# Optimization experiments

Measured on AMD Instinct MI355X. Metric: run time of the kernel, lower is better.

## Reference

```python
import jax, jax.numpy as jnp
import numpy as np

SCOPE = 27
IN_CHANNELS = 512
RICKER_WIDTH = 4.0
DAMP = 0.12
N, H, W = 16, 56, 56


def mexican_hat(scope, width, damping, self_connect=False):
    # Ricker (mexican hat) wavelet sampled at integer offsets around the center.
    t = jnp.arange(scope, dtype=jnp.float32) - (scope - 1) / 2.0
    norm = 2.0 / (np.sqrt(3.0 * width) * np.pi ** 0.25)
    w = damping * norm * (1.0 - (t / width) ** 2) * jnp.exp(-(t ** 2) / (2.0 * width ** 2))
    if not self_connect:
        w = w.at[scope // 2].set(0.0)  # zero self-connection at the center tap
    return w


def setup_inputs() -> dict:
    key = jax.random.key(0)
    activations = jax.random.normal(key, (N, IN_CHANNELS, H, W), dtype=jnp.float32)
    inhibition_filter = mexican_hat(SCOPE, RICKER_WIDTH, DAMP, self_connect=False)
    return {"activations": activations, "inhibition_filter": inhibition_filter}


def reference(activations, inhibition_filter):
    # Converged inhibition: solve y = x + k (circ-conv over channels) y, i.e.
    # y = F^-1( F(x) / F(delta - k_padded) ), FFT taken along the channel axis.
    C = activations.shape[1]
    scope = inhibition_filter.shape[0]
    # pad_roll: zero-pad the scope-length kernel to C taps, then roll so the
    # kernel center sits at circular position 0.
    k = jnp.pad(inhibition_filter, (0, C - scope))
    k = jnp.roll(k, -(scope // 2))
    delta = jnp.zeros((C,), dtype=activations.dtype).at[0].set(1.0)
    fk = jnp.fft.fft(delta - k)                      # complex [C]
    fx = jnp.fft.fft(activations, axis=1)            # complex [N,C,H,W]
    y = jnp.fft.ifft(fx / fk[None, :, None, None], axis=1).real
    return y.astype(activations.dtype)
```

## Files before the change

kernel.cpp:

```cpp
#include <hip/hip_runtime.h>
#include <cstdint>
#include <cstddef>

#define CCH   512
#define FSCOPE 27
#define HWSP  3136
#define NBATCH 16
#define NCOL  (NBATCH*HWSP)

#define BM 128
#define BN 128
#define BK 64
#define NKT (CCH/BK)

#define PI_F 3.14159265358979323846f

typedef __bf16 bf16x8 __attribute__((ext_vector_type(8)));
typedef float  f32x4  __attribute__((ext_vector_type(4)));

static __device__ __forceinline__ unsigned short f2bf(float f) {
  unsigned u = __builtin_bit_cast(unsigned, f);
  unsigned r = 0x7FFFu + ((u >> 16) & 1u);
  return (unsigned short)((u + r) >> 16);
}

__global__ __launch_bounds__(512)
void k_h2(const float* __restrict__ w, float* __restrict__ h) {
  __shared__ float red[8];
  const int d = blockIdx.x;
  const int m = threadIdx.x;

  float re = 1.0f, im = 0.0f;
  #pragma unroll
  for (int j = 0; j < FSCOPE; ++j) {
    int t = (m * (j - FSCOPE/2)) % CCH;
    if (t < 0) t += CCH;
    float ang = (2.0f * PI_F / CCH) * (float)t;
    float s, c;
    sincosf(ang, &s, &c);
    float wj = w[j];
    re -= wj * c;
    im += wj * s;
  }

  int t = (m * d) & (CCH - 1);
  float ang = (2.0f * PI_F / CCH) * (float)t;
  float s, c;
  sincosf(ang, &s, &c);
  float inv = 1.0f / (re * re + im * im);
  float term = (c * re + s * im) * inv;

  #pragma unroll
  for (int off = 32; off > 0; off >>= 1)
    term += __shfl_down(term, off, 64);

  const int lane = m & 63, wv = m >> 6;
  if (lane == 0) red[wv] = term;
  __syncthreads();
  if (m == 0) {
    float tot = 0.f;
    #pragma unroll
    for (int i = 0; i < 8; ++i) tot += red[i];
    h[d] = tot / (float)CCH;
  }
}

__global__ void k_buildH(const float* __restrict__ h, unsigned short* __restrict__ Hm) {
  int m = blockIdx.x;
  for (int k = threadIdx.x; k < CCH; k += blockDim.x) {
    Hm[m*CCH + k] = f2bf(h[(m - k) & (CCH - 1)]);
  }
}

__global__ __launch_bounds__(256, 4)
void k_gemm(const float* __restrict__ X, const unsigned short* __restrict__ Hm,
            float* __restrict__ Y) {
  __shared__ __align__(16) unsigned char lds[BM*BK*2 + BN*BK*2];

  const int tid  = threadIdx.x;
  const int lane = tid & 63;
  const int w    = tid >> 6;

  int bid = blockIdx.x;
  int cpx = gridDim.x >> 3;
  int swz = (bid & 7) * cpx + (bid >> 3);
  const int tm = swz & 3;
  const int tc = swz >> 2;

  const int m0 = tm * BM;
  const int j0 = tc * BN;

  unsigned char* Al = lds;
  unsigned char* Bl = lds + BM*BK*2;

  const int fg = tid & 31;
  const int kg = tid >> 5;
  const int jb = j0 + fg*4;
  const int nb = jb / HWSP;
  const int sb = jb - nb * HWSP;
  const float* Xb = X + (size_t)nb * (CCH*(size_t)HWSP) + sb;

  int wrOff[4];
  #pragma unroll
  for (int c = 0; c < 4; ++c) {
    int col = fg*4 + c;
    int g = (col & 7) ^ ((col >> 3) & 7);
    wrOff[c] = col*128 + (((kg ^ g) & 7) << 4);
  }

  const int wr = w >> 1, wc = w & 1;
  int aBase[4], aSw[4], bBase[4], bSw[4];
  #pragma unroll
  for (int fm = 0; fm < 4; ++fm) {
    int m = wr*64 + fm*16 + (lane & 15);
    aBase[fm] = m*128;
    aSw[fm]   = (m & 7) << 4;
  }
  #pragma unroll
  for (int fn = 0; fn < 4; ++fn) {
    int col = wc*64 + fn*16 + (lane & 15);
    bBase[fn] = col*128;
    bSw[fn]   = ((col & 7) ^ ((col >> 3) & 7)) << 4;
  }

  f32x4 acc[4][4];
  #pragma unroll
  for (int i = 0; i < 4; ++i)
    #pragma unroll
    for (int j = 0; j < 4; ++j)
      acc[i][j] = (f32x4){0.f, 0.f, 0.f, 0.f};

  for (int kt = 0; kt < NKT; ++kt) {
    float4 bv[8];
    const float* Xk = Xb + (size_t)(kt*BK + kg*8) * HWSP;
    #pragma unroll
    for (int kk = 0; kk < 8; ++kk)
      bv[kk] = *reinterpret_cast<const float4*>(Xk + (size_t)kk * HWSP);

    if (kt > 0) __syncthreads();

    #pragma unroll
    for (int i = 0; i < 4; ++i) {
      int m0w = w*32 + i*8;
      int m   = m0w + (lane >> 3);
      int c   = lane & 7;
      const unsigned short* src =
          Hm + (size_t)(m0 + m) * CCH + kt*BK + 8*(c ^ (m & 7));
      unsigned char* dst = Al + m0w * 128;
      __builtin_amdgcn_global_load_lds(
          (const __attribute__((address_space(1))) void*)src,
          (__attribute__((address_space(3))) void*)dst, 16, 0, 0);
    }

    #pragma unroll
    for (int c = 0; c < 4; ++c) {
      union { __bf16 h[8]; int4 v; } u;
      #pragma unroll
      for (int kk = 0; kk < 8; ++kk) {
        float f = (c==0) ? bv[kk].x : (c==1) ? bv[kk].y : (c==2) ? bv[kk].z : bv[kk].w;
        u.h[kk] = (__bf16)f;
      }
      *reinterpret_cast<int4*>(Bl + wrOff[c]) = u.v;
    }

    __syncthreads();

    #pragma unroll
    for (int ks = 0; ks < 2; ++ks) {
      const int kbyte = ks*64 + ((lane >> 4) << 4);
      bf16x8 af[4], bfr[4];
      #pragma unroll
      for (int fm = 0; fm < 4; ++fm)
        af[fm] = *reinterpret_cast<const bf16x8*>(Al + aBase[fm] + (kbyte ^ aSw[fm]));
      #pragma unroll
      for (int fn = 0; fn < 4; ++fn)
        bfr[fn] = *reinterpret_cast<const bf16x8*>(Bl + bBase[fn] + (kbyte ^ bSw[fn]));
      #pragma unroll
      for (int fm = 0; fm < 4; ++fm)
        #pragma unroll
        for (int fn = 0; fn < 4; ++fn)
          acc[fm][fn] = __builtin_amdgcn_mfma_f32_16x16x32_bf16(
              af[fm], bfr[fn], acc[fm][fn], 0, 0, 0);
    }
  }

  #pragma unroll
  for (int fn = 0; fn < 4; ++fn) {
    int colg = j0 + wc*64 + fn*16 + (lane & 15);
    int n = colg / HWSP;
    int s = colg - n * HWSP;
    float* Yb = Y + (size_t)n * (CCH*(size_t)HWSP) + s;
    #pragma unroll
    for (int fm = 0; fm < 4; ++fm) {
      int mrow = m0 + wr*64 + fm*16 + ((lane >> 4) << 2);
      #pragma unroll
      for (int r = 0; r < 4; ++r)
        Yb[(size_t)(mrow + r) * HWSP] = acc[fm][fn][r];
    }
  }
}

extern "C" void kernel_launch(void* const* d_in, const int* in_sizes, int n_in,
                              void* d_out, int out_size, void* d_ws, size_t ws_size,
                              hipStream_t stream) {
  const float* X = (const float*)d_in[0];
  const float* w = (const float*)d_in[1];
  float* Y = (float*)d_out;

  float* h           = (float*)d_ws;
  unsigned short* Hm = (unsigned short*)((char*)d_ws + 4096);

  k_h2    <<<CCH, 512, 0, stream>>>(w, h);
  k_buildH<<<CCH, 256, 0, stream>>>(h, Hm);

  const int nblk = (CCH/BM) * (NCOL/BN);
  k_gemm  <<<nblk, 256, 0, stream>>>(X, Hm, Y);
}
```

Measured before the change: 65.31 us.

## Double-buffer GEMM LDS tiles with register prefetch of next K-tile

Converts the GEMM main loop to a double-buffered LDS scheme. The next K-tile of both the circulant matrix and the activations is loaded into registers before the current tile's MFMAs run, then stored into the alternate buffer, so there is one barrier per iteration instead of two. The A-tile load changes from global_load_lds direct-to-LDS to register loads followed by swizzled LDS stores. LDS grows to 64KB and the occupancy hint drops from 4 to 2 blocks per CU, trading occupancy-based latency hiding for explicit overlap and adding register pressure.

New measurement: 80.94 us. +23.9%, slower.

```diff
diff --git a/kernel.cpp b/kernel.cpp
--- a/kernel.cpp
+++ b/kernel.cpp
@@ -72,10 +72,10 @@
   }
 }
 
-__global__ __launch_bounds__(256, 4)
+__global__ __launch_bounds__(256, 2)
 void k_gemm(const float* __restrict__ X, const unsigned short* __restrict__ Hm,
             float* __restrict__ Y) {
-  __shared__ __align__(16) unsigned char lds[BM*BK*2 + BN*BK*2];
+  __shared__ __align__(16) unsigned char lds[65536];
 
   const int tid  = threadIdx.x;
   const int lane = tid & 63;
@@ -90,8 +90,10 @@
   const int m0 = tm * BM;
   const int j0 = tc * BN;
 
-  unsigned char* Al = lds;
-  unsigned char* Bl = lds + BM*BK*2;
+  const int ar = tid >> 3;
+  const int ac = tid & 7;
+  const unsigned short* aSrcBase = Hm + (size_t)(m0 + ar) * CCH + ac * 8;
+  const int aWr0 = ar * 128 + ((ac ^ (ar & 7)) << 4);
 
   const int fg = tid & 31;
   const int kg = tid >> 5;
@@ -130,28 +132,20 @@
     for (int j = 0; j < 4; ++j)
       acc[i][j] = (f32x4){0.f, 0.f, 0.f, 0.f};
 
-  for (int kt = 0; kt < NKT; ++kt) {
+  {
+    int4 av[4];
     float4 bv[8];
-    const float* Xk = Xb + (size_t)(kt*BK + kg*8) * HWSP;
+    #pragma unroll
+    for (int i = 0; i < 4; ++i)
+      av[i] = *reinterpret_cast<const int4*>(aSrcBase + (size_t)i * 32 * CCH);
+    const float* Xk = Xb + (size_t)(kg * 8) * HWSP;
     #pragma unroll
     for (int kk = 0; kk < 8; ++kk)
       bv[kk] = *reinterpret_cast<const float4*>(Xk + (size_t)kk * HWSP);
 
-    if (kt > 0) __syncthreads();
-
-    #pragma unroll
-    for (int i = 0; i < 4; ++i) {
-      int m0w = w*32 + i*8;
-      int m   = m0w + (lane >> 3);
-      int c   = lane & 7;
-      const unsigned short* src =
-          Hm + (size_t)(m0 + m) * CCH + kt*BK + 8*(c ^ (m & 7));
-      unsigned char* dst = Al + m0w * 128;
-      __builtin_amdgcn_global_load_lds(
-          (const __attribute__((address_space(1))) void*)src,
-          (__attribute__((address_space(3))) void*)dst, 16, 0, 0);
-    }
-
+    #pragma unroll
+    for (int i = 0; i < 4; ++i)
+      *reinterpret_cast<int4*>(lds + aWr0 + i * 4096) = av[i];
     #pragma unroll
     for (int c = 0; c < 4; ++c) {
       union { __bf16 h[8]; int4 v; } u;
@@ -160,10 +154,32 @@
         float f = (c==0) ? bv[kk].x : (c==1) ? bv[kk].y : (c==2) ? bv[kk].z : bv[kk].w;
         u.h[kk] = (__bf16)f;
       }
-      *reinterpret_cast<int4*>(Bl + wrOff[c]) = u.v;
-    }
-
-    __syncthreads();
+      *reinterpret_cast<int4*>(lds + 32768 + wrOff[c]) = u.v;
+    }
+  }
+  __syncthreads();
+
+  #pragma unroll 2
+  for (int kt = 0; kt < NKT; ++kt) {
+    const int cur   = kt & 1;
+    const int aoffC = cur * 16384;
+    const int boffC = 32768 + cur * 16384;
+    const int aoffN = 16384 - aoffC;
+    const int boffN = 32768 + (16384 - aoffC);
+
+    int4 av[4];
+    float4 bv[8];
+    const bool pf = (kt + 1 < NKT);
+    if (pf) {
+      const unsigned short* as = aSrcBase + (kt + 1) * BK;
+      #pragma unroll
+      for (int i = 0; i < 4; ++i)
+        av[i] = *reinterpret_cast<const int4*>(as + (size_t)i * 32 * CCH);
+      const float* Xk = Xb + (size_t)((kt + 1) * BK + kg * 8) * HWSP;
+      #pragma unroll
+      for (int kk = 0; kk < 8; ++kk)
+        bv[kk] = *reinterpret_cast<const float4*>(Xk + (size_t)kk * HWSP);
+    }
 
     #pragma unroll
     for (int ks = 0; ks < 2; ++ks) {
@@ -171,10 +187,10 @@
       bf16x8 af[4], bfr[4];
       #pragma unroll
       for (int fm = 0; fm < 4; ++fm)
-        af[fm] = *reinterpret_cast<const bf16x8*>(Al + aBase[fm] + (kbyte ^ aSw[fm]));
+        af[fm] = *reinterpret_cast<const bf16x8*>(lds + aoffC + aBase[fm] + (kbyte ^ aSw[fm]));
       #pragma unroll
       for (int fn = 0; fn < 4; ++fn)
-        bfr[fn] = *reinterpret_cast<const bf16x8*>(Bl + bBase[fn] + (kbyte ^ bSw[fn]));
+        bfr[fn] = *reinterpret_cast<const bf16x8*>(lds + boffC + bBase[fn] + (kbyte ^ bSw[fn]));
       #pragma unroll
       for (int fm = 0; fm < 4; ++fm)
         #pragma unroll
@@ -182,6 +198,24 @@
           acc[fm][fn] = __builtin_amdgcn_mfma_f32_16x16x32_bf16(
               af[fm], bfr[fn], acc[fm][fn], 0, 0, 0);
     }
+
+    if (pf) {
+      #pragma unroll
+      for (int i = 0; i < 4; ++i)
+        *reinterpret_cast<int4*>(lds + aoffN + aWr0 + i * 4096) = av[i];
+      #pragma unroll
+      for (int c = 0; c < 4; ++c) {
+        union { __bf16 h[8]; int4 v; } u;
+        #pragma unroll
+        for (int kk = 0; kk < 8; ++kk) {
+          float f = (c==0) ? bv[kk].x : (c==1) ? bv[kk].y : (c==2) ? bv[kk].z : bv[kk].w;
+          u.h[kk] = (__bf16)f;
+        }
+        *reinterpret_cast<int4*>(lds + boffN + wrOff[c]) = u.v;
+      }
+    }
+
+    __syncthreads();
   }
 
   #pragma unroll
```

## Software-pipeline GEMM mainloop with double-buffered A tile and register-prefetched B

Applied to the files above, without the earlier changes.

The GEMM mainloop now prefetches the next K-tile while computing the current one. The Hm (A) tile is loaded directly into a second LDS buffer, and the X (B) values are loaded into registers, then converted to bf16 and written to LDS after the MFMAs. The aim is to hide global-load latency behind compute. In exchange, LDS grows to 48KB and the occupancy hint of 4 blocks is dropped, which may lower occupancy and raise register pressure.

After: 59.91 us, median of 2. -8.3%, faster.

```diff
diff --git a/kernel.cpp b/kernel.cpp
--- a/kernel.cpp
+++ b/kernel.cpp
@@ -72,10 +72,10 @@
   }
 }
 
-__global__ __launch_bounds__(256, 4)
+__global__ __launch_bounds__(256)
 void k_gemm(const float* __restrict__ X, const unsigned short* __restrict__ Hm,
             float* __restrict__ Y) {
-  __shared__ __align__(16) unsigned char lds[BM*BK*2 + BN*BK*2];
+  __shared__ __align__(16) unsigned char lds[49152];
 
   const int tid  = threadIdx.x;
   const int lane = tid & 63;
@@ -90,8 +90,7 @@
   const int m0 = tm * BM;
   const int j0 = tc * BN;
 
-  unsigned char* Al = lds;
-  unsigned char* Bl = lds + BM*BK*2;
+  unsigned char* Bl = lds + 32768;
 
   const int fg = tid & 31;
   const int kg = tid >> 5;
@@ -123,6 +122,9 @@
     bSw[fn]   = ((col & 7) ^ ((col >> 3) & 7)) << 4;
   }
 
+  const int aRow = lane >> 3;
+  const int aChk = lane & 7;
+
   f32x4 acc[4][4];
   #pragma unroll
   for (int i = 0; i < 4; ++i)
@@ -130,40 +132,54 @@
     for (int j = 0; j < 4; ++j)
       acc[i][j] = (f32x4){0.f, 0.f, 0.f, 0.f};
 
+  float4 bv[8];
+
+  #pragma unroll
+  for (int i = 0; i < 4; ++i) {
+    int m0w = w*32 + i*8;
+    int m   = m0w + aRow;
+    const unsigned short* src =
+        Hm + (size_t)(m0 + m) * CCH + 8*(aChk ^ (m & 7));
+    __builtin_amdgcn_global_load_lds(
+        (const __attribute__((address_space(1))) void*)src,
+        (__attribute__((address_space(3))) void*)(lds + m0w*128), 16, 0, 0);
+  }
+  #pragma unroll
+  for (int kk = 0; kk < 8; ++kk)
+    bv[kk] = *reinterpret_cast<const float4*>(Xb + (size_t)(kg*8 + kk) * HWSP);
+  __syncthreads();
+  #pragma unroll
+  for (int c = 0; c < 4; ++c) {
+    union { __bf16 h[8]; int4 v; } u;
+    #pragma unroll
+    for (int kk = 0; kk < 8; ++kk) {
+      float f = (c==0) ? bv[kk].x : (c==1) ? bv[kk].y : (c==2) ? bv[kk].z : bv[kk].w;
+      u.h[kk] = (__bf16)f;
+    }
+    *reinterpret_cast<int4*>(Bl + wrOff[c]) = u.v;
+  }
+  __syncthreads();
+
   for (int kt = 0; kt < NKT; ++kt) {
-    float4 bv[8];
-    const float* Xk = Xb + (size_t)(kt*BK + kg*8) * HWSP;
-    #pragma unroll
-    for (int kk = 0; kk < 8; ++kk)
-      bv[kk] = *reinterpret_cast<const float4*>(Xk + (size_t)kk * HWSP);
-
-    if (kt > 0) __syncthreads();
-
-    #pragma unroll
-    for (int i = 0; i < 4; ++i) {
-      int m0w = w*32 + i*8;
-      int m   = m0w + (lane >> 3);
-      int c   = lane & 7;
-      const unsigned short* src =
-          Hm + (size_t)(m0 + m) * CCH + kt*BK + 8*(c ^ (m & 7));
-      unsigned char* dst = Al + m0w * 128;
-      __builtin_amdgcn_global_load_lds(
-          (const __attribute__((address_space(1))) void*)src,
-          (__attribute__((address_space(3))) void*)dst, 16, 0, 0);
-    }
-
-    #pragma unroll
-    for (int c = 0; c < 4; ++c) {
-      union { __bf16 h[8]; int4 v; } u;
-      #pragma unroll
-      for (int kk = 0; kk < 8; ++kk) {
-        float f = (c==0) ? bv[kk].x : (c==1) ? bv[kk].y : (c==2) ? bv[kk].z : bv[kk].w;
-        u.h[kk] = (__bf16)f;
+    const int aoffC = (kt & 1) * 16384;
+    const int aoffN = 16384 - aoffC;
+
+    if (kt + 1 < NKT) {
+      #pragma unroll
+      for (int i = 0; i < 4; ++i) {
+        int m0w = w*32 + i*8;
+        int m   = m0w + aRow;
+        const unsigned short* src =
+            Hm + (size_t)(m0 + m) * CCH + (kt + 1)*BK + 8*(aChk ^ (m & 7));
+        __builtin_amdgcn_global_load_lds(
+            (const __attribute__((address_space(1))) void*)src,
+            (__attribute__((address_space(3))) void*)(lds + aoffN + m0w*128), 16, 0, 0);
       }
-      *reinterpret_cast<int4*>(Bl + wrOff[c]) = u.v;
-    }
-
-    __syncthreads();
+      const float* Xk = Xb + (size_t)((kt + 1)*BK + kg*8) * HWSP;
+      #pragma unroll
+      for (int kk = 0; kk < 8; ++kk)
+        bv[kk] = *reinterpret_cast<const float4*>(Xk + (size_t)kk * HWSP);
+    }
 
     #pragma unroll
     for (int ks = 0; ks < 2; ++ks) {
@@ -171,7 +187,7 @@
       bf16x8 af[4], bfr[4];
       #pragma unroll
       for (int fm = 0; fm < 4; ++fm)
-        af[fm] = *reinterpret_cast<const bf16x8*>(Al + aBase[fm] + (kbyte ^ aSw[fm]));
+        af[fm] = *reinterpret_cast<const bf16x8*>(lds + aoffC + aBase[fm] + (kbyte ^ aSw[fm]));
       #pragma unroll
       for (int fn = 0; fn < 4; ++fn)
         bfr[fn] = *reinterpret_cast<const bf16x8*>(Bl + bBase[fn] + (kbyte ^ bSw[fn]));
@@ -181,6 +197,22 @@
         for (int fn = 0; fn < 4; ++fn)
           acc[fm][fn] = __builtin_amdgcn_mfma_f32_16x16x32_bf16(
               af[fm], bfr[fn], acc[fm][fn], 0, 0, 0);
+    }
+
+    __syncthreads();
+
+    if (kt + 1 < NKT) {
+      #pragma unroll
+      for (int c = 0; c < 4; ++c) {
+        union { __bf16 h[8]; int4 v; } u;
+        #pragma unroll
+        for (int kk = 0; kk < 8; ++kk) {
+          float f = (c==0) ? bv[kk].x : (c==1) ? bv[kk].y : (c==2) ? bv[kk].z : bv[kk].w;
+          u.h[kk] = (__bf16)f;
+        }
+        *reinterpret_cast<int4*>(Bl + wrOff[c]) = u.v;
+      }
+      __syncthreads();
     }
   }
 
```
